# Kernel tuning notes

Measured on AMD Instinct MI355X. Metric: run time of the kernel, lower is better.

## Reference

```python
import jax, jax.numpy as jnp
import numpy as np

HIDDEN = 2560
NUM_HEADS = 80
HEAD_DIM = 64
STATE = 128
N_GROUPS = 1
CONV_K = 4
CHUNK = 256
INTER = 2 * HIDDEN                       # 5120 = NUM_HEADS * HEAD_DIM
CONV_DIM = INTER + 2 * N_GROUPS * STATE  # 5376
PROJ = INTER + CONV_DIM + NUM_HEADS      # 10576
EPS = 1e-5
DT_MIN, DT_MAX = 0.0, 100.0


def segment_sum(x):
    # x: (..., T) -> (..., T, T); out[i, j] = sum_{j < k <= i} x[k], -inf above diag
    T = x.shape[-1]
    xe = jnp.broadcast_to(x[..., :, None], x.shape + (T,))  # [i, j] = x[i]
    mask_lo = jnp.tril(jnp.ones((T, T), dtype=bool), -1)
    seg = jnp.cumsum(jnp.where(mask_lo, xe, 0.0), axis=-2)
    mask = jnp.tril(jnp.ones((T, T), dtype=bool), 0)
    return jnp.where(mask, seg, -jnp.inf)


def setup_inputs() -> dict:
    key = jax.random.key(0)
    k0, k1, k2, k3 = jax.random.split(key, 4)
    x = jax.random.normal(k0, (2, 2048, HIDDEN), jnp.float32)
    in_proj_w = jax.random.normal(k1, (PROJ, HIDDEN), jnp.float32) * (HIDDEN ** -0.5)
    conv1d_w = jax.random.normal(k2, (CONV_DIM, CONV_K), jnp.float32) * (CONV_K ** -0.5)
    conv1d_b = jnp.zeros((CONV_DIM,), jnp.float32)
    A_log = jnp.log(jnp.arange(1, NUM_HEADS + 1, dtype=jnp.float32))
    D = jnp.ones((NUM_HEADS,), jnp.float32)
    dt_bias = jnp.ones((NUM_HEADS,), jnp.float32)
    norm_weight = jnp.ones((INTER,), jnp.float32)
    out_proj_w = jax.random.normal(k3, (HIDDEN, INTER), jnp.float32) * (INTER ** -0.5)
    return dict(input_states=x, in_proj_w=in_proj_w, conv1d_w=conv1d_w,
                conv1d_b=conv1d_b, A_log=A_log, D=D, dt_bias=dt_bias,
                norm_weight=norm_weight, out_proj_w=out_proj_w)


def _mamba2_forward(input_states, in_proj_w, conv1d_w, conv1d_b, A_log, D,
                    dt_bias, norm_weight, out_proj_w):
    b, s, _ = input_states.shape
    proj = input_states @ in_proj_w.T                       # (b, s, PROJ)
    gate, hs, dt = jnp.split(proj, [INTER, INTER + CONV_DIM], axis=-1)

    # causal depthwise conv1d + SiLU
    xT = jnp.transpose(hs, (0, 2, 1))                       # (b, conv_dim, s)
    xT = jnp.pad(xT, ((0, 0), (0, 0), (CONV_K - 1, 0)))
    conv = jax.lax.conv_general_dilated(
        xT, conv1d_w[:, None, :], (1,), 'VALID',
        feature_group_count=CONV_DIM, dimension_numbers=('NCH', 'OIH', 'NCH'))
    hs = jax.nn.silu(jnp.transpose(conv + conv1d_b[None, :, None], (0, 2, 1)))

    hs, B, C = jnp.split(hs, [INTER, INTER + N_GROUPS * STATE], axis=-1)
    A = -jnp.exp(A_log)                                     # (h,)
    dt = jnp.clip(jax.nn.softplus(dt + dt_bias), DT_MIN, DT_MAX)  # (b, s, h)

    X = hs.reshape(b, s, NUM_HEADS, HEAD_DIM)
    rep = NUM_HEADS // N_GROUPS
    B = jnp.repeat(B.reshape(b, s, N_GROUPS, STATE), rep, axis=2)
    C = jnp.repeat(C.reshape(b, s, N_GROUPS, STATE), rep, axis=2)

    pad = (-s) % CHUNK
    D_res = D[None, None, :, None] * jnp.pad(X, ((0, 0), (0, pad), (0, 0), (0, 0)))
    Xd = X * dt[..., None]                                  # discretized input
    dA = A[None, None, :] * dt                              # (b, s, h)

    def chunk(t):
        t = jnp.pad(t, [(0, 0), (0, pad)] + [(0, 0)] * (t.ndim - 2))
        return t.reshape(t.shape[0], -1, CHUNK, *t.shape[2:])

    Xc, Bc, Cc = chunk(Xd), chunk(B), chunk(C)              # (b, c, l, h, ...)
    Ac = jnp.transpose(chunk(dA), (0, 3, 1, 2))             # (b, h, c, l)
    A_cum = jnp.cumsum(Ac, axis=-1)

    # 1. intra-chunk (diagonal block) outputs
    L = jnp.exp(segment_sum(Ac))                            # (b, h, c, l, l)
    G = jnp.einsum('bclhn,bcshn->bhcls', Cc, Bc)
    Y_diag = jnp.einsum('bhcls,bcshp->bclhp', G * L, Xc)

    # 2. per-chunk final states
    decay_states = jnp.exp(A_cum[..., -1:] - A_cum)         # (b, h, c, l)
    states = jnp.einsum('bclhn,bhcl,bclhp->bchpn', Bc, decay_states, Xc)

    # 3. inter-chunk recurrence
    A_last = A_cum[..., -1]                                 # (b, h, c)
    decay_chunk = jnp.exp(segment_sum(jnp.pad(A_last, ((0, 0), (0, 0), (1, 0)))))
    states = jnp.concatenate([jnp.zeros_like(states[:, :1]), states], axis=1)
    new_states = jnp.einsum('bhzc,bchpn->bzhpn', decay_chunk, states)
    states = new_states[:, :-1]                             # (b, c, h, p, n)

    # 4. state -> output conversion
    Y_off = jnp.einsum('bclhn,bchpn,bhcl->bclhp', Cc, states, jnp.exp(A_cum))

    y = (Y_diag + Y_off).reshape(b, -1, NUM_HEADS, HEAD_DIM) + D_res
    y = y[:, :s].reshape(b, s, INTER)

    # gated RMSNorm
    y = y * jax.nn.silu(gate)
    var = jnp.mean(y * y, axis=-1, keepdims=True)
    y = y * jax.lax.rsqrt(var + EPS) * norm_weight
    return y @ out_proj_w.T


def reference(input_states, in_proj_w, conv1d_w, conv1d_b, A_log, D, dt_bias,
              norm_weight, out_proj_w):
    return _mamba2_forward(input_states, in_proj_w, conv1d_w, conv1d_b, A_log,
                           D, dt_bias, norm_weight, out_proj_w)
```

## Files before the change

kernel.cpp:

```cpp
#include <hip/hip_runtime.h>
#include <hip/hip_bf16.h>
#include <math.h>

#define HIDDEN   2560
#define NUM_HEADS 80
#define HEAD_DIM 64
#define STATE    128
#define CONV_K   4
#define CHUNK    256
#define INTER    (2*HIDDEN)
#define CONV_DIM (INTER + 2*STATE)
#define PROJ     (INTER + CONV_DIM + NUM_HEADS)
#define PROJ_PAD 10240
#define NBC      336
#define NBCP     384
#define EPS      1e-5f

#define BATCH 2
#define SEQ   2048
#define TOK   (BATCH*SEQ)
#define NC    (SEQ/CHUNK)
#define KSPL2 8
#define KCH2  (HIDDEN/KSPL2)

typedef __attribute__((ext_vector_type(8))) short bf16x8;
typedef __attribute__((ext_vector_type(4))) float f32x4;

#define MFMA16(a,b,c) __builtin_amdgcn_mfma_f32_16x16x32_bf16((a),(b),(c),0,0,0)

__device__ __forceinline__ unsigned short f2bf(float f){
    union{float f;unsigned u;}v; v.f=f;
    unsigned r = v.u + 0x7fffu + ((v.u>>16)&1u);
    return (unsigned short)(r>>16);
}
__device__ __forceinline__ float bf2f(unsigned short s){
    union{unsigned u;float f;}v; v.u = ((unsigned)s)<<16; return v.f;
}
__device__ __forceinline__ void unpack8(uint4 u, float* e){
    e[0]=bf2f((unsigned short)(u.x&0xffff)); e[1]=bf2f((unsigned short)(u.x>>16));
    e[2]=bf2f((unsigned short)(u.y&0xffff)); e[3]=bf2f((unsigned short)(u.y>>16));
    e[4]=bf2f((unsigned short)(u.z&0xffff)); e[5]=bf2f((unsigned short)(u.z>>16));
    e[6]=bf2f((unsigned short)(u.w&0xffff)); e[7]=bf2f((unsigned short)(u.w>>16));
}

__device__ __forceinline__ void gld16(const void* g, void* l){
    __builtin_amdgcn_global_load_lds((const __attribute__((address_space(1))) void*)g,
                                     (__attribute__((address_space(3))) void*)l, 16, 0, 0);
}

template<bool BF16OUT>
__global__ __launch_bounds__(256) void gemm_bf16(const unsigned short* __restrict__ A, int lda,
                                                 const unsigned short* __restrict__ B, int ldb,
                                                 void* __restrict__ Cv, int ldc, int K) {
    __shared__ unsigned short As[128][64];
    __shared__ unsigned short Bs[128][64];
    int tid = threadIdx.x;
    int lane = tid & 63, wid = tid >> 6;
    int wr = wid >> 1, wc = wid & 1;

    int bm, bn;
    if ((gridDim.y & 7) == 0) {
        int bid   = blockIdx.y * gridDim.x + blockIdx.x;
        int xcd   = bid & 7;
        int local = bid >> 3;
        int mrows = gridDim.y >> 3;
        bm = (xcd * mrows + (local % mrows)) * 128;
        bn = (local / mrows) * 128;
    } else {
        bm = blockIdx.y * 128;
        bn = blockIdx.x * 128;
    }

    f32x4 acc[4][4];
    #pragma unroll
    for (int i=0;i<4;i++)
        #pragma unroll
        for (int j=0;j<4;j++) acc[i][j] = (f32x4){0.f,0.f,0.f,0.f};

    int srow_off = lane >> 3;
    int sslot    = lane & 7;

    for (int k0 = 0; k0 < K; k0 += 64) {
        #pragma unroll
        for (int q=0;q<4;q++){
            int brow = (wid*4+q)*8;
            int row  = brow + srow_off;
            int sl   = sslot ^ (row & 7);
            gld16(A + (size_t)(bm + row)*lda + k0 + sl*8, &As[brow][0]);
            gld16(B + (size_t)(bn + row)*ldb + k0 + sl*8, &Bs[brow][0]);
        }
        __syncthreads();
        #pragma unroll
        for (int kk=0; kk<64; kk+=32){
            bf16x8 a[4], b[4];
            #pragma unroll
            for (int i=0;i<4;i++){
                int row = wr*64 + i*16 + (lane&15);
                int slot = ((kk>>3) + (lane>>4)) ^ (row & 7);
                a[i] = *(const bf16x8*)&As[row][slot*8];
            }
            #pragma unroll
            for (int j=0;j<4;j++){
                int row = wc*64 + j*16 + (lane&15);
                int slot = ((kk>>3) + (lane>>4)) ^ (row & 7);
                b[j] = *(const bf16x8*)&Bs[row][slot*8];
            }
            #pragma unroll
            for (int i=0;i<4;i++)
                #pragma unroll
                for (int j=0;j<4;j++)
                    acc[i][j] = MFMA16(a[i], b[j], acc[i][j]);
        }
        __syncthreads();
    }
    #pragma unroll
    for (int i=0;i<4;i++){
        int row0 = bm + wr*64 + i*16 + (lane>>4)*4;
        #pragma unroll
        for (int j=0;j<4;j++){
            int col = bn + wc*64 + j*16 + (lane&15);
            #pragma unroll
            for (int r=0;r<4;r++){
                if (BF16OUT)
                    ((unsigned short*)Cv)[(size_t)(row0+r)*ldc + col] = f2bf(acc[i][j][r]);
                else
                    ((float*)Cv)[(size_t)(row0+r)*ldc + col] = acc[i][j][r];
            }
        }
    }
}

__global__ __launch_bounds__(256) void bc_splitk_mfma(const unsigned short* __restrict__ xhi,
                                                      const unsigned short* __restrict__ xlo,
                                                      const unsigned short* __restrict__ whi,
                                                      const unsigned short* __restrict__ wlo,
                                                      float* __restrict__ Cpart) {
    __shared__ unsigned short As[128][64];
    __shared__ unsigned short Bs[128][64];
    int tid = threadIdx.x;
    int lane = tid & 63, wid = tid >> 6;
    int wr = wid >> 1, wc = wid & 1;
    int bn = blockIdx.x * 128, bm = blockIdx.y * 128, z = blockIdx.z;

    f32x4 acc[4][4];
    #pragma unroll
    for (int i=0;i<4;i++)
        #pragma unroll
        for (int j=0;j<4;j++) acc[i][j] = (f32x4){0.f,0.f,0.f,0.f};

    int srow_off = lane >> 3;
    int sslot    = lane & 7;

    for (int term = 0; term < 3; ++term){
        const unsigned short* A = (term==2) ? xlo : xhi;
        const unsigned short* B = (term==0) ? wlo : whi;
        for (int k0 = z*KCH2; k0 < z*KCH2 + KCH2; k0 += 64) {
            #pragma unroll
            for (int q=0;q<4;q++){
                int brow = (wid*4+q)*8;
                int row  = brow + srow_off;
                int sl   = sslot ^ (row & 7);
                gld16(A + (size_t)(bm + row)*HIDDEN + k0 + sl*8, &As[brow][0]);
                gld16(B + (size_t)(bn + row)*HIDDEN + k0 + sl*8, &Bs[brow][0]);
            }
            __syncthreads();
            #pragma unroll
            for (int kk=0; kk<64; kk+=32){
                bf16x8 a[4], b[4];
                #pragma unroll
                for (int i=0;i<4;i++){
                    int row = wr*64 + i*16 + (lane&15);
                    int slot = ((kk>>3) + (lane>>4)) ^ (row & 7);
                    a[i] = *(const bf16x8*)&As[row][slot*8];
                }
                #pragma unroll
                for (int j=0;j<4;j++){
                    int row = wc*64 + j*16 + (lane&15);
                    int slot = ((kk>>3) + (lane>>4)) ^ (row & 7);
                    b[j] = *(const bf16x8*)&Bs[row][slot*8];
                }
                #pragma unroll
                for (int i=0;i<4;i++)
                    #pragma unroll
                    for (int j=0;j<4;j++)
                        acc[i][j] = MFMA16(a[i], b[j], acc[i][j]);
            }
            __syncthreads();
        }
    }
    float* Cz = Cpart + (size_t)z*TOK*NBCP;
    #pragma unroll
    for (int i=0;i<4;i++){
        int row0 = bm + wr*64 + i*16 + (lane>>4)*4;
        #pragma unroll
        for (int j=0;j<4;j++){
            int col = bn + wc*64 + j*16 + (lane&15);
            #pragma unroll
            for (int r=0;r<4;r++)
                Cz[(size_t)(row0+r)*NBCP + col] = acc[i][j][r];
        }
    }
}

__global__ __launch_bounds__(256) void reduce_bc2(const float* __restrict__ part,
                                                  const float* __restrict__ dt_bias,
                                                  float* __restrict__ outBC,
                                                  float* __restrict__ dtbuf) {
    size_t i4 = (size_t)blockIdx.x*256 + threadIdx.x;
    if (i4 >= (size_t)TOK*NBCP/4) return;
    size_t i = i4*4;
    float4 s = *(const float4*)(part + i);
    #pragma unroll
    for (int z=1; z<KSPL2; z++){
        float4 v = *(const float4*)(part + (size_t)z*TOK*NBCP + i);
        s.x += v.x; s.y += v.y; s.z += v.z; s.w += v.w;
    }
    int col = (int)(i % NBCP);
    int t   = (int)(i / NBCP);
    if (col < 256) {
        *(float4*)(outBC + (size_t)t*NBC + col) = s;
    } else if (col < NBC) {
        int h = col - 256;
        float e[4] = {s.x, s.y, s.z, s.w};
        #pragma unroll
        for (int u=0;u<4;u++){
            float xv = e[u] + dt_bias[h+u];
            float sp = (xv > 20.f) ? xv : log1pf(expf(xv));
            e[u] = fminf(fmaxf(sp, 0.f), 100.f);
        }
        float4 o; o.x=e[0]; o.y=e[1]; o.z=e[2]; o.w=e[3];
        *(float4*)(dtbuf + (size_t)t*NUM_HEADS + h) = o;
    }
}

#define N4A ((size_t)TOK*HIDDEN/4)
#define N4B ((size_t)PROJ_PAD*HIDDEN/4)
#define N4C ((size_t)NBCP*HIDDEN/4)
__global__ __launch_bounds__(256) void prep_kernel(const float* __restrict__ x,
                                                   const float* __restrict__ in_w,
                                                   unsigned short* __restrict__ xhi,
                                                   unsigned short* __restrict__ xlo,
                                                   unsigned short* __restrict__ w1b,
                                                   unsigned short* __restrict__ wbc_hi,
                                                   unsigned short* __restrict__ wbc_lo) {
    size_t gid = (size_t)blockIdx.x*256 + threadIdx.x;
    if (gid < N4A) {
        size_t i = gid*4;
        float4 v = *(const float4*)(x + i);
        float e[4] = {v.x, v.y, v.z, v.w};
        ushort4 h, l;
        unsigned short* hp = (unsigned short*)&h;
        unsigned short* lp = (unsigned short*)&l;
        #pragma unroll
        for (int u=0;u<4;u++){
            unsigned short hv = f2bf(e[u]);
            hp[u] = hv;
            lp[u] = f2bf(e[u] - bf2f(hv));
        }
        *(ushort4*)(xhi + i) = h;
        *(ushort4*)(xlo + i) = l;
    } else if (gid < N4A + N4B) {
        size_t i = (gid - N4A)*4;
        float4 v = *(const float4*)(in_w + i);
        ushort4 o;
        o.x=f2bf(v.x); o.y=f2bf(v.y); o.z=f2bf(v.z); o.w=f2bf(v.w);
        *(ushort4*)(w1b + i) = o;
    } else {
        size_t j = gid - N4A - N4B;
        size_t i = j*4;
        int row = (int)(i / HIDDEN);
        int kk  = (int)(i % HIDDEN);
        ushort4 h, l;
        h.x=h.y=h.z=h.w=0; l.x=l.y=l.z=l.w=0;
        if (row < NBC){
            float4 v = *(const float4*)(in_w + (size_t)(2*INTER + row)*HIDDEN + kk);
            float e[4] = {v.x, v.y, v.z, v.w};
            unsigned short* hp = (unsigned short*)&h;
            unsigned short* lp = (unsigned short*)&l;
            #pragma unroll
            for (int u=0;u<4;u++){
                unsigned short hv = f2bf(e[u]);
                hp[u] = hv;
                lp[u] = f2bf(e[u] - bf2f(hv));
            }
        }
        *(ushort4*)(wbc_hi + i) = h;
        *(ushort4*)(wbc_lo + i) = l;
    }
}

#define XBLK ((TOK/64)*(INTER/64))
#define W2BLK ((int)(((size_t)HIDDEN*INTER/4)/256))
__global__ __launch_bounds__(256) void conv_fused(const unsigned short* __restrict__ projb,
                                                  const float* __restrict__ projBC,
                                                  const float* __restrict__ cw,
                                                  const float* __restrict__ cb,
                                                  const float* __restrict__ out_w,
                                                  unsigned short* __restrict__ XT,
                                                  float* __restrict__ xBC_BC,
                                                  unsigned short* __restrict__ BT,
                                                  unsigned short* __restrict__ Cb,
                                                  unsigned short* __restrict__ w2b) {
    __shared__ unsigned short raw[68][66];
    int bid = blockIdx.x;
    int tid = threadIdx.x;
    if (bid < XBLK) {
        int bx = bid & 63, by = bid >> 6;
        int t0 = bx * 64, d0 = by * 64;
        int b  = t0 / SEQ;
        int s0 = t0 % SEQ;
        for (int f = tid; f < 67*8; f += 256){
            int r = f >> 3, g = f & 7;
            int sp = s0 - 3 + r;
            uint4 v;
            if (sp >= 0) v = *(const uint4*)(projb + ((size_t)(b*SEQ+sp))*PROJ_PAD + INTER + d0 + g*8);
            else { v.x=0u; v.y=0u; v.z=0u; v.w=0u; }
            unsigned int* dst = (unsigned int*)&raw[r][g*8];
            dst[0]=v.x; dst[1]=v.y; dst[2]=v.z; dst[3]=v.w;
        }
        __syncthreads();
        int t = tid & 63, dg = tid >> 6;
        #pragma unroll
        for (int dd = 0; dd < 16; dd++){
            int d = dg*16 + dd;
            float acc = cb[d0+d];
            #pragma unroll
            for (int j=0;j<CONV_K;j++)
                acc += cw[(d0+d)*CONV_K+j] * bf2f(raw[t+j][d]);
            float val = acc/(1.f+expf(-acc));
            XT[((size_t)(b*INTER + d0 + d))*SEQ + s0 + t] = f2bf(val);
        }
    } else if (bid < XBLK + TOK) {
        int idx = (bid - XBLK)*256 + tid;
        int d = idx & 255;
        int t = idx >> 8;
        int b = t / SEQ, sl = t % SEQ;
        int dc = INTER + d;
        float acc = cb[dc];
        #pragma unroll
        for (int j=0;j<CONV_K;j++){
            int sp = sl - (CONV_K-1) + j;
            if (sp >= 0)
                acc += cw[dc*CONV_K+j] * projBC[((size_t)(b*SEQ+sp))*NBC + d];
        }
        float val = acc / (1.f + expf(-acc));
        xBC_BC[(size_t)t*256 + d] = val;
        if (d < 128)
            BT[((size_t)(b*128 + d))*SEQ + sl] = f2bf(val);
        else
            Cb[(size_t)t*128 + (d-128)] = f2bf(val);
    } else {
        size_t i4 = (size_t)(bid - XBLK - TOK)*256 + tid;
        size_t i = i4*4;
        float4 v = *(const float4*)(out_w + i);
        ushort4 o; o.x=f2bf(v.x); o.y=f2bf(v.y); o.z=f2bf(v.z); o.w=f2bf(v.w);
        *(ushort4*)(w2b + i) = o;
    }
}

__global__ __launch_bounds__(256) void cumsum_kernel(const float* __restrict__ dtbuf,
                                                     const float* __restrict__ A_log,
                                                     float* __restrict__ A_cum) {
    int c = blockIdx.x, h = blockIdx.y, b = blockIdx.z;
    int l = threadIdx.x;
    float A = -expf(A_log[h]);
    float v = A * dtbuf[(size_t)(b*SEQ + c*CHUNK + l)*NUM_HEADS + h];
    __shared__ float buf[CHUNK];
    buf[l] = v;
    __syncthreads();
    for (int off=1; off<CHUNK; off<<=1){
        float t = (l>=off) ? buf[l-off] : 0.f;
        __syncthreads();
        buf[l] += t;
        __syncthreads();
    }
    A_cum[((size_t)b*NUM_HEADS + h)*SEQ + c*CHUNK + l] = buf[l];
}

__global__ __launch_bounds__(256) void g_kernel(const float* __restrict__ xBC_BC,
                                                unsigned short* __restrict__ G) {
    int c = blockIdx.x, p = blockIdx.y, b = blockIdx.z;
    int lt = 0, a0 = 0;
    while (a0 + lt + 1 <= p) { a0 += lt + 1; lt++; }
    int st = p - a0;
    int l0 = lt*32, s0 = st*32;
    __shared__ float Cs[32][132];
    __shared__ float Bs[32][132];
    int tid = threadIdx.x, ty = tid >> 4, tx = tid & 15;
    float acc[2][2];
    acc[0][0]=0.f; acc[0][1]=0.f; acc[1][0]=0.f; acc[1][1]=0.f;

    size_t rowC = ((size_t)(b*SEQ + c*CHUNK + l0))*256 + 128;
    size_t rowB = ((size_t)(b*SEQ + c*CHUNK + s0))*256;
    #pragma unroll
    for (int it=0; it<4; it++){
        int f = tid + it*256;
        int r = f >> 5, c4 = f & 31;
        *(float4*)&Cs[r][c4*4] = *(const float4*)(xBC_BC + rowC + (size_t)r*256 + c4*4);
        *(float4*)&Bs[r][c4*4] = *(const float4*)(xBC_BC + rowB + (size_t)r*256 + c4*4);
    }
    __syncthreads();
    #pragma unroll 8
    for (int k=0;k<128;k++){
        float a0v = Cs[ty*2][k],   a1v = Cs[ty*2+1][k];
        float b0v = Bs[tx*2][k],   b1v = Bs[tx*2+1][k];
        acc[0][0] += a0v*b0v; acc[0][1] += a0v*b1v;
        acc[1][0] += a1v*b0v; acc[1][1] += a1v*b1v;
    }
    size_t Gb = ((size_t)(b*NC + c)) << 16;
    #pragma unroll
    for (int i=0;i<2;i++){
        ushort2 g2;
        g2.x = f2bf(acc[i][0]); g2.y = f2bf(acc[i][1]);
        *(ushort2*)(G + Gb + (size_t)(l0 + ty*2 + i)*256 + s0 + tx*2) = g2;
    }
}

__global__ __launch_bounds__(256) void states_mfma(const unsigned short* __restrict__ XT,
                                                   const unsigned short* __restrict__ BT,
                                                   const float* __restrict__ dtbuf,
                                                   const float* __restrict__ A_cum,
                                                   unsigned short* __restrict__ statesT) {
    int c = blockIdx.x, h = blockIdx.y, b = blockIdx.z;
    __shared__ unsigned short Asx[64][64];
    __shared__ unsigned short Bs[128][64];
    __shared__ float wl[CHUNK];
    int tid = threadIdx.x, lane = tid & 63, wid = tid >> 6;
    {
        const float* ac = A_cum + ((size_t)(b*NUM_HEADS+h))*SEQ + c*CHUNK;
        float Alast = ac[CHUNK-1];
        wl[tid] = expf(Alast - ac[tid]) * dtbuf[((size_t)(b*SEQ + c*CHUNK + tid))*NUM_HEADS + h];
    }
    __syncthreads();
    f32x4 acc[4][2];
    #pragma unroll
    for (int i=0;i<4;i++)
        #pragma unroll
        for (int j=0;j<2;j++) acc[i][j] = (f32x4){0.f,0.f,0.f,0.f};

    for (int kc = 0; kc < 4; kc++){
        int lbase = kc*64;
        #pragma unroll
        for (int q=0;q<4;q++){
            int brow = (wid*4+q)*8;
            int row  = brow + (lane>>3);
            int sl   = (lane&7) ^ (row & 7);
            gld16(BT + ((size_t)(b*128 + row))*SEQ + c*CHUNK + lbase + sl*8, &Bs[brow][0]);
        }
        #pragma unroll
        for (int it=0; it<2; it++){
            int f = tid + it*256;
            int r = f >> 3, g = f & 7;
            uint4 v = *(const uint4*)(XT + ((size_t)(b*INTER + h*HEAD_DIM + r))*SEQ + c*CHUNK + lbase + g*8);
            float e[8]; unpack8(v, e);
            unsigned short o[8];
            #pragma unroll
            for (int u=0;u<8;u++) o[u] = f2bf(e[u] * wl[lbase + g*8 + u]);
            int slot = g ^ (r & 7);
            *(ushort4*)&Asx[r][slot*8]   = *(ushort4*)&o[0];
            *(ushort4*)&Asx[r][slot*8+4] = *(ushort4*)&o[4];
        }
        __syncthreads();
        #pragma unroll
        for (int kk=0; kk<64; kk+=32){
            bf16x8 a[4], bb[2];
            #pragma unroll
            for (int i=0;i<4;i++){
                int row = i*16 + (lane&15);
                int slot = ((kk>>3)+(lane>>4)) ^ (row&7);
                a[i] = *(const bf16x8*)&Asx[row][slot*8];
            }
            #pragma unroll
            for (int j=0;j<2;j++){
                int row = wid*32 + j*16 + (lane&15);
                int slot = ((kk>>3)+(lane>>4)) ^ (row&7);
                bb[j] = *(const bf16x8*)&Bs[row][slot*8];
            }
            #pragma unroll
            for (int i=0;i<4;i++)
                #pragma unroll
                for (int j=0;j<2;j++)
                    acc[i][j] = MFMA16(a[i], bb[j], acc[i][j]);
        }
        __syncthreads();
    }
    size_t sb = ((size_t)((b*NC + c)*NUM_HEADS + h))*(HEAD_DIM*STATE);
    #pragma unroll
    for (int i=0;i<4;i++){
        #pragma unroll
        for (int j=0;j<2;j++){
            int n = wid*32 + j*16 + (lane&15);
            int p0 = i*16 + (lane>>4)*4;
            #pragma unroll
            for (int r=0;r<4;r++)
                statesT[sb + (size_t)(p0+r)*128 + n] = f2bf(acc[i][j][r]);
        }
    }
}

__global__ __launch_bounds__(256) void recur_kernel(const float* __restrict__ A_cum,
                                                    unsigned short* __restrict__ states) {
    int h = blockIdx.x, b = blockIdx.y, z = blockIdx.z;
    int tid = threadIdx.x;
    float Srun[8];
    #pragma unroll
    for (int i=0;i<8;i++) Srun[i]=0.f;
    const float* acum = A_cum + ((size_t)b*NUM_HEADS + h)*SEQ;
    for (int c=0;c<NC;c++){
        float alast = acum[c*CHUNK + CHUNK-1];
        float dec = expf(alast);
        size_t base = ((size_t)((b*NC + c)*NUM_HEADS + h))*(HEAD_DIM*STATE);
        #pragma unroll
        for (int i=0;i<8;i++){
            size_t idx = base + (size_t)tid + (size_t)(z*8+i)*256;
            float raw = bf2f(states[idx]);
            states[idx] = f2bf(Srun[i]);
            Srun[i] = Srun[i]*dec + raw;
        }
    }
}

__global__ __launch_bounds__(256) void yscan_mfma(const unsigned short* __restrict__ G,
                                                  const unsigned short* __restrict__ Cb,
                                                  const unsigned short* __restrict__ XT,
                                                  const float* __restrict__ dtbuf,
                                                  const float* __restrict__ A_cum,
                                                  const unsigned short* __restrict__ statesT,
                                                  const float* __restrict__ Dvec,
                                                  unsigned short* __restrict__ projb) {
    int xb = blockIdx.x;
    int c = xb & 7, lt = xb >> 3;
    int h = blockIdx.y, b = blockIdx.z;
    int l0 = lt*64;
    __shared__ __align__(16) char pool[32768];
    unsigned short (*Cs)[128] = (unsigned short(*)[128])pool;
    unsigned short (*St)[128] = (unsigned short(*)[128])(pool + 16384);
    unsigned short (*Gw)[64]  = (unsigned short(*)[64])pool;
    unsigned short (*Xs)[64]  = (unsigned short(*)[64])(pool + 8192);
    float (*Ot)[68]           = (float(*)[68])pool;
    __shared__ float ac[CHUNK], dts[CHUNK];
    int tid = threadIdx.x, lane = tid & 63, wid = tid >> 6;
    ac[tid]  = A_cum[((size_t)(b*NUM_HEADS + h))*SEQ + c*CHUNK + tid];
    dts[tid] = dtbuf[((size_t)(b*SEQ + c*CHUNK + tid))*NUM_HEADS + h];

    size_t stb = ((size_t)((b*NC + c)*NUM_HEADS + h))*(HEAD_DIM*STATE);
    #pragma unroll
    for (int q=0;q<4;q++){
        int brow = (wid*4+q)*4;
        int row  = brow + (lane>>4);
        int sl   = (lane&15) ^ (row & 7);
        gld16(Cb + ((size_t)(b*SEQ + c*CHUNK + l0 + row))*128 + sl*8, &Cs[brow][0]);
        gld16(statesT + stb + (size_t)row*128 + sl*8, &St[brow][0]);
    }
    __syncthreads();

    f32x4 acc1[4];
    #pragma unroll
    for (int j=0;j<4;j++) acc1[j] = (f32x4){0.f,0.f,0.f,0.f};
    #pragma unroll
    for (int kk=0; kk<128; kk+=32){
        int arow = wid*16 + (lane&15);
        int aslot = ((kk>>3)+(lane>>4)) ^ (arow&7);
        bf16x8 a = *(const bf16x8*)&Cs[arow][aslot*8];
        #pragma unroll
        for (int j=0;j<4;j++){
            int brow = j*16 + (lane&15);
            int bslot = ((kk>>3)+(lane>>4)) ^ (brow&7);
            bf16x8 bb = *(const bf16x8*)&St[brow][bslot*8];
            acc1[j] = MFMA16(a, bb, acc1[j]);
        }
    }
    float el[4];
    #pragma unroll
    for (int r=0;r<4;r++) el[r] = expf(ac[l0 + wid*16 + (lane>>4)*4 + r]);
    float master[4][4];
    #pragma unroll
    for (int j=0;j<4;j++)
        #pragma unroll
        for (int r=0;r<4;r++) master[j][r] = acc1[j][r]*el[r];
    __syncthreads();

    size_t Gb = ((size_t)(b*NC + c)) << 16;
    f32x4 acc2[4];
    #pragma unroll
    for (int j=0;j<4;j++) acc2[j] = (f32x4){0.f,0.f,0.f,0.f};
    for (int st=0; st<=lt; st++){
        int s0 = st*64;
        #pragma unroll
        for (int it=0; it<2; it++){
            int f = tid + it*256;
            int r = f >> 3, g = f & 7;
            uint4 v = *(const uint4*)(G + Gb + (size_t)(l0 + r)*256 + s0 + g*8);
            float e[8]; unpack8(v, e);
            float acl = ac[l0 + r];
            unsigned short o[8];
            #pragma unroll
            for (int u=0;u<8;u++){
                int s = s0 + g*8 + u;
                float w = (s <= l0 + r) ? expf(acl - ac[s])*dts[s] : 0.f;
                o[u] = f2bf(e[u]*w);
            }
            int slot = g ^ (r&7);
            *(ushort4*)&Gw[r][slot*8]   = *(ushort4*)&o[0];
            *(ushort4*)&Gw[r][slot*8+4] = *(ushort4*)&o[4];
        }
        #pragma unroll
        for (int q=0;q<2;q++){
            int brow = (wid*2+q)*8;
            int row  = brow + (lane>>3);
            int sl   = (lane&7) ^ (row&7);
            gld16(XT + ((size_t)(b*INTER + h*HEAD_DIM + row))*SEQ + c*CHUNK + s0 + sl*8,
                  &Xs[brow][0]);
        }
        __syncthreads();
        #pragma unroll
        for (int kk=0; kk<64; kk+=32){
            int arow = wid*16 + (lane&15);
            int aslot = ((kk>>3)+(lane>>4)) ^ (arow&7);
            bf16x8 a = *(const bf16x8*)&Gw[arow][aslot*8];
            #pragma unroll
            for (int j=0;j<4;j++){
                int brow = j*16 + (lane&15);
                int bslot = ((kk>>3)+(lane>>4)) ^ (brow&7);
                bf16x8 bb = *(const bf16x8*)&Xs[brow][bslot*8];
                acc2[j] = MFMA16(a, bb, acc2[j]);
            }
        }
        if (st < lt) __syncthreads();
    }

    float Dh = Dvec[h];
    #pragma unroll
    for (int j=0;j<4;j++){
        int p = j*16 + (lane&15);
        #pragma unroll
        for (int r=0;r<4;r++){
            int sl_ = wid*16 + (lane>>4)*4 + r;
            int slot = (sl_>>3) ^ (p&7);
            float xv = bf2f(Xs[p][slot*8 + (sl_&7)]);
            master[j][r] += acc2[j][r] + Dh*xv;
        }
    }
    __syncthreads();

    #pragma unroll
    for (int j=0;j<4;j++){
        int p = j*16 + (lane&15);
        #pragma unroll
        for (int r=0;r<4;r++)
            Ot[wid*16 + (lane>>4)*4 + r][p] = master[j][r];
    }
    __syncthreads();
    #pragma unroll
    for (int it=0; it<4; it++){
        int f = tid + it*256;
        int r = f >> 4, c4 = f & 15;
        ushort4 o;
        o.x = f2bf(Ot[r][c4*4+0]); o.y = f2bf(Ot[r][c4*4+1]);
        o.z = f2bf(Ot[r][c4*4+2]); o.w = f2bf(Ot[r][c4*4+3]);
        *(ushort4*)(projb + ((size_t)(b*SEQ + c*CHUNK + l0 + r))*PROJ_PAD + INTER + h*HEAD_DIM + c4*4) = o;
    }
}

__global__ __launch_bounds__(256) void gate_norm_kernel(const unsigned short* __restrict__ projb,
                                                        const float* __restrict__ normw,
                                                        unsigned short* __restrict__ yb) {
    int t = blockIdx.x;
    int tid = threadIdx.x;
    const unsigned short* row = projb + (size_t)t*PROJ_PAD;
    __shared__ float red[4];
    float vals[20];
    float ss = 0.f;
    #pragma unroll
    for (int i=0;i<5;i++){
        int j = (tid + i*256)*4;
        ushort4 g4 = *(const ushort4*)(row + j);
        ushort4 y4 = *(const ushort4*)(row + INTER + j);
        #pragma unroll
        for (int u=0;u<4;u++){
            float g = bf2f(((const unsigned short*)&g4)[u]);
            float y = bf2f(((const unsigned short*)&y4)[u]);
            float gv = g / (1.f + expf(-g));
            float v = y * gv;
            vals[i*4+u] = v;
            ss += v*v;
        }
    }
    #pragma unroll
    for (int off=32; off; off>>=1) ss += __shfl_xor(ss, off);
    if ((tid&63)==0) red[tid>>6] = ss;
    __syncthreads();
    float tot = red[0]+red[1]+red[2]+red[3];
    float inv = rsqrtf(tot/(float)INTER + EPS);
    #pragma unroll
    for (int i=0;i<5;i++){
        int j = (tid + i*256)*4;
        ushort4 o;
        o.x = f2bf(vals[i*4+0] * inv * normw[j+0]);
        o.y = f2bf(vals[i*4+1] * inv * normw[j+1]);
        o.z = f2bf(vals[i*4+2] * inv * normw[j+2]);
        o.w = f2bf(vals[i*4+3] * inv * normw[j+3]);
        *(ushort4*)(yb + (size_t)t*INTER + j) = o;
    }
}

extern "C" void kernel_launch(void* const* d_in, const int* in_sizes, int n_in,
                              void* d_out, int out_size, void* d_ws, size_t ws_size,
                              hipStream_t stream) {
    const float* x        = (const float*)d_in[0];
    const float* in_w     = (const float*)d_in[1];
    const float* conv_w   = (const float*)d_in[2];
    const float* conv_b   = (const float*)d_in[3];
    const float* A_log    = (const float*)d_in[4];
    const float* Dvec     = (const float*)d_in[5];
    const float* dt_bias  = (const float*)d_in[6];
    const float* norm_w   = (const float*)d_in[7];
    const float* out_w    = (const float*)d_in[8];
    float* out = (float*)d_out;
    (void)ws_size; (void)n_in; (void)in_sizes; (void)out_size;

    const size_t PROJB   = (size_t)TOK*PROJ_PAD*2;
    const size_t PROJBCB = (size_t)TOK*NBC*4;
    const size_t XTB     = (size_t)TOK*INTER*2;
    const size_t XBCBCB  = (size_t)TOK*256*4;
    const size_t BTB     = (size_t)BATCH*128*SEQ*2;
    const size_t CBB     = (size_t)TOK*128*2;
    const size_t GBYTES  = (size_t)BATCH*NC*CHUNK*CHUNK*2;
    const size_t DTB     = (size_t)TOK*NUM_HEADS*4;
    const size_t ACUMB   = DTB;
    const size_t STB     = (size_t)BATCH*NC*NUM_HEADS*HEAD_DIM*STATE*2;
    const size_t XHB   = (size_t)TOK*HIDDEN*2;
    const size_t WBCB  = (size_t)NBCP*HIDDEN*2;
    const size_t YBB   = (size_t)TOK*INTER*2;

    char* base = (char*)d_ws;
    size_t off = 0;
    unsigned short* projb  = (unsigned short*)(base + off); off += PROJB;
    float* projBC          = (float*)(base + off);          off += PROJBCB;
    unsigned short* XTp    = (unsigned short*)(base + off); off += XTB;
    float* xBC_BC          = (float*)(base + off);          off += XBCBCB;
    unsigned short* BTp    = (unsigned short*)(base + off); off += BTB;
    unsigned short* Cbp    = (unsigned short*)(base + off); off += CBB;
    unsigned short* Gp     = (unsigned short*)(base + off); off += GBYTES;
    float* dtbuf           = (float*)(base + off);          off += DTB;
    float* A_cum           = (float*)(base + off);          off += ACUMB;
    unsigned short* statesT= (unsigned short*)(base + off); off += STB;
    char*  T               = base + off;
    unsigned short* xhi    = (unsigned short*)T;
    unsigned short* xlo    = (unsigned short*)(T + XHB);
    unsigned short* wbc_hi = (unsigned short*)(T + 2*XHB);
    unsigned short* wbc_lo = (unsigned short*)(T + 2*XHB + WBCB);
    unsigned short* w1b    = (unsigned short*)(T + 2*XHB + 2*WBCB);
    float* bcpart          = (float*)w1b;
    unsigned short* yb     = (unsigned short*)T;
    unsigned short* w2b    = (unsigned short*)(T + YBB);

    {
        unsigned total_blocks = (unsigned)((N4A + N4B + N4C) / 256);
        prep_kernel<<<total_blocks, 256, 0, stream>>>(x, in_w, xhi, xlo, w1b, wbc_hi, wbc_lo);
    }
    gemm_bf16<true><<<dim3(PROJ_PAD/128, TOK/128), 256, 0, stream>>>(xhi, HIDDEN, w1b, HIDDEN,
                                                                     projb, PROJ_PAD, HIDDEN);
    bc_splitk_mfma<<<dim3(NBCP/128, TOK/128, KSPL2), 256, 0, stream>>>(xhi, xlo, wbc_hi, wbc_lo, bcpart);
    reduce_bc2<<<(unsigned)(((size_t)TOK*NBCP/4)/256), 256, 0, stream>>>(bcpart, dt_bias, projBC, dtbuf);
    conv_fused<<<XBLK + TOK + W2BLK, 256, 0, stream>>>(projb, projBC, conv_w, conv_b, out_w,
                                                       XTp, xBC_BC, BTp, Cbp, w2b);
    cumsum_kernel<<<dim3(NC, NUM_HEADS, BATCH), 256, 0, stream>>>(dtbuf, A_log, A_cum);
    g_kernel<<<dim3(NC, 36, BATCH), 256, 0, stream>>>(xBC_BC, Gp);
    states_mfma<<<dim3(NC, NUM_HEADS, BATCH), 256, 0, stream>>>(XTp, BTp, dtbuf, A_cum, statesT);
    recur_kernel<<<dim3(NUM_HEADS, BATCH, 4), 256, 0, stream>>>(A_cum, statesT);
    yscan_mfma<<<dim3(NC*4, NUM_HEADS, BATCH), 256, 0, stream>>>(Gp, Cbp, XTp, dtbuf, A_cum,
                                                                 statesT, Dvec, projb);
    gate_norm_kernel<<<TOK, 256, 0, stream>>>(projb, norm_w, yb);
    gemm_bf16<false><<<dim3(HIDDEN/128, TOK/128), 256, 0, stream>>>(yb, INTER, w2b, INTER,
                                                                    out, HIDDEN, INTER);
}
```

Measured before the change: 710.3 us.

## Merge independent pipeline stages into horizontally fused mega-kernels

Combines independent kernels into shared launches that branch on block index: the main in-projection GEMM with the split-K BC GEMM, the split-K reduction with the conv over the x channels, the BC conv with the cumsum and the out-weight conversion, and the states computation with the G kernel. The GEMM1 epilogue now stages output tiles through shared memory so the stores are coalesced 16-byte writes. This cuts launch count and lets small kernels fill the tail of larger ones. The cost is heavier, branchy kernels whose register and LDS use is set by the largest branch, which may lower occupancy.

```diff
diff --git a/kernel.cpp b/kernel.cpp
--- a/kernel.cpp
+++ b/kernel.cpp
@@ -23,37 +23,183 @@
 #define KSPL2 8
 #define KCH2  (HIDDEN/KSPL2)
 
+#define G1_BLOCKS 2560
+#define BC_BLOCKS 768
+#define RED_BLOCKS 1536
+#define CXT_BLOCKS 5120
+#define CBC_BLOCKS 4096
+#define CUM_BLOCKS 1280
+#define W2_BLOCKS  12800
+#define ST_BLOCKS  1280
+#define GK_BLOCKS  576
+
 typedef __attribute__((ext_vector_type(8))) short bf16x8;
 typedef __attribute__((ext_vector_type(4))) float f32x4;
+typedef unsigned short us;
 
 #define MFMA16(a,b,c) __builtin_amdgcn_mfma_f32_16x16x32_bf16((a),(b),(c),0,0,0)
 
-__device__ __forceinline__ unsigned short f2bf(float f){
+__device__ __forceinline__ us f2bf(float f){
     union{float f;unsigned u;}v; v.f=f;
     unsigned r = v.u + 0x7fffu + ((v.u>>16)&1u);
-    return (unsigned short)(r>>16);
-}
-__device__ __forceinline__ float bf2f(unsigned short s){
+    return (us)(r>>16);
+}
+__device__ __forceinline__ float bf2f(us s){
     union{unsigned u;float f;}v; v.u = ((unsigned)s)<<16; return v.f;
 }
 __device__ __forceinline__ void unpack8(uint4 u, float* e){
-    e[0]=bf2f((unsigned short)(u.x&0xffff)); e[1]=bf2f((unsigned short)(u.x>>16));
-    e[2]=bf2f((unsigned short)(u.y&0xffff)); e[3]=bf2f((unsigned short)(u.y>>16));
-    e[4]=bf2f((unsigned short)(u.z&0xffff)); e[5]=bf2f((unsigned short)(u.z>>16));
-    e[6]=bf2f((unsigned short)(u.w&0xffff)); e[7]=bf2f((unsigned short)(u.w>>16));
-}
-
+    e[0]=bf2f((us)(u.x&0xffff)); e[1]=bf2f((us)(u.x>>16));
+    e[2]=bf2f((us)(u.y&0xffff)); e[3]=bf2f((us)(u.y>>16));
+    e[4]=bf2f((us)(u.z&0xffff)); e[5]=bf2f((us)(u.z>>16));
+    e[6]=bf2f((us)(u.w&0xffff)); e[7]=bf2f((us)(u.w>>16));
+}
 __device__ __forceinline__ void gld16(const void* g, void* l){
     __builtin_amdgcn_global_load_lds((const __attribute__((address_space(1))) void*)g,
                                      (__attribute__((address_space(3))) void*)l, 16, 0, 0);
 }
 
+__global__ __launch_bounds__(256) void mega_gemm1_bc(const us* __restrict__ xhi,
+                                                     const us* __restrict__ xlo,
+                                                     const us* __restrict__ w1b,
+                                                     const us* __restrict__ wbc_hi,
+                                                     const us* __restrict__ wbc_lo,
+                                                     us* __restrict__ projb,
+                                                     float* __restrict__ Cpart) {
+    __shared__ __align__(16) char SH[32768];
+    us (*As)[64] = (us(*)[64])SH;
+    us (*Bs)[64] = (us(*)[64])(SH + 16384);
+    int bid = blockIdx.x;
+    int tid = threadIdx.x;
+    int lane = tid & 63, wid = tid >> 6;
+    int wr = wid >> 1, wc = wid & 1;
+    int srow_off = lane >> 3;
+    int sslot    = lane & 7;
+
+    f32x4 acc[4][4];
+    #pragma unroll
+    for (int i=0;i<4;i++)
+        #pragma unroll
+        for (int j=0;j<4;j++) acc[i][j] = (f32x4){0.f,0.f,0.f,0.f};
+
+    if (bid < G1_BLOCKS) {
+        int xcd = bid & 7, local = bid >> 3;
+        int bm = (xcd*4 + (local & 3))*128;
+        int bn = (local >> 2)*128;
+        for (int k0 = 0; k0 < HIDDEN; k0 += 64) {
+            #pragma unroll
+            for (int q=0;q<4;q++){
+                int brow = (wid*4+q)*8;
+                int row  = brow + srow_off;
+                int sl   = sslot ^ (row & 7);
+                gld16(xhi + (size_t)(bm + row)*HIDDEN + k0 + sl*8, &As[brow][0]);
+                gld16(w1b + (size_t)(bn + row)*HIDDEN + k0 + sl*8, &Bs[brow][0]);
+            }
+            __syncthreads();
+            #pragma unroll
+            for (int kk=0; kk<64; kk+=32){
+                bf16x8 a[4], b[4];
+                #pragma unroll
+                for (int i=0;i<4;i++){
+                    int row = wr*64 + i*16 + (lane&15);
+                    int slot = ((kk>>3) + (lane>>4)) ^ (row & 7);
+                    a[i] = *(const bf16x8*)&As[row][slot*8];
+                }
+                #pragma unroll
+                for (int j=0;j<4;j++){
+                    int row = wc*64 + j*16 + (lane&15);
+                    int slot = ((kk>>3) + (lane>>4)) ^ (row & 7);
+                    b[j] = *(const bf16x8*)&Bs[row][slot*8];
+                }
+                #pragma unroll
+                for (int i=0;i<4;i++)
+                    #pragma unroll
+                    for (int j=0;j<4;j++)
+                        acc[i][j] = MFMA16(a[i], b[j], acc[i][j]);
+            }
+            __syncthreads();
+        }
+        us (*Ct)[128] = (us(*)[128])SH;
+        #pragma unroll
+        for (int i=0;i<4;i++){
+            int r0 = wr*64 + i*16 + (lane>>4)*4;
+            #pragma unroll
+            for (int j=0;j<4;j++){
+                int cc = wc*64 + j*16 + (lane&15);
+                #pragma unroll
+                for (int r=0;r<4;r++)
+                    Ct[r0+r][cc] = f2bf(acc[i][j][r]);
+            }
+        }
+        __syncthreads();
+        #pragma unroll
+        for (int it=0; it<8; it++){
+            int f = tid + it*256;
+            int row = f >> 4, ch = f & 15;
+            *(uint4*)(projb + (size_t)(bm+row)*PROJ_PAD + bn + ch*8) = *(uint4*)&Ct[row][ch*8];
+        }
+    } else {
+        int b2 = bid - G1_BLOCKS;
+        int bn = (b2 % 3)*128;
+        int bm = ((b2/3) & 31)*128;
+        int z  = b2 / 96;
+        for (int term = 0; term < 3; ++term){
+            const us* A = (term==2) ? xlo : xhi;
+            const us* B = (term==0) ? wbc_lo : wbc_hi;
+            for (int k0 = z*KCH2; k0 < z*KCH2 + KCH2; k0 += 64) {
+                #pragma unroll
+                for (int q=0;q<4;q++){
+                    int brow = (wid*4+q)*8;
+                    int row  = brow + srow_off;
+                    int sl   = sslot ^ (row & 7);
+                    gld16(A + (size_t)(bm + row)*HIDDEN + k0 + sl*8, &As[brow][0]);
+                    gld16(B + (size_t)(bn + row)*HIDDEN + k0 + sl*8, &Bs[brow][0]);
+                }
+                __syncthreads();
+                #pragma unroll
+                for (int kk=0; kk<64; kk+=32){
+                    bf16x8 a[4], b[4];
+                    #pragma unroll
+                    for (int i=0;i<4;i++){
+                        int row = wr*64 + i*16 + (lane&15);
+                        int slot = ((kk>>3) + (lane>>4)) ^ (row & 7);
+                        a[i] = *(const bf16x8*)&As[row][slot*8];
+                    }
+                    #pragma unroll
+                    for (int j=0;j<4;j++){
+                        int row = wc*64 + j*16 + (lane&15);
+                        int slot = ((kk>>3) + (lane>>4)) ^ (row & 7);
+                        b[j] = *(const bf16x8*)&Bs[row][slot*8];
+                    }
+                    #pragma unroll
+                    for (int i=0;i<4;i++)
+                        #pragma unroll
+                        for (int j=0;j<4;j++)
+                            acc[i][j] = MFMA16(a[i], b[j], acc[i][j]);
+                }
+                __syncthreads();
+            }
+        }
+        float* Cz = Cpart + (size_t)z*TOK*NBCP;
+        #pragma unroll
+        for (int i=0;i<4;i++){
+            int row0 = bm + wr*64 + i*16 + (lane>>4)*4;
+            #pragma unroll
+            for (int j=0;j<4;j++){
+                int col = bn + wc*64 + j*16 + (lane&15);
+                #pragma unroll
+                for (int r=0;r<4;r++)
+                    Cz[(size_t)(row0+r)*NBCP + col] = acc[i][j][r];
+            }
+        }
+    }
+}
+
 template<bool BF16OUT>
-__global__ __launch_bounds__(256) void gemm_bf16(const unsigned short* __restrict__ A, int lda,
-                                                 const unsigned short* __restrict__ B, int ldb,
+__global__ __launch_bounds__(256) void gemm_bf16(const us* __restrict__ A, int lda,
+                                                 const us* __restrict__ B, int ldb,
                                                  void* __restrict__ Cv, int ldc, int K) {
-    __shared__ unsigned short As[128][64];
-    __shared__ unsigned short Bs[128][64];
+    __shared__ us As[128][64];
+    __shared__ us Bs[128][64];
     int tid = threadIdx.x;
     int lane = tid & 63, wid = tid >> 6;
     int wr = wid >> 1, wc = wid & 1;
@@ -122,114 +268,11 @@
             #pragma unroll
             for (int r=0;r<4;r++){
                 if (BF16OUT)
-                    ((unsigned short*)Cv)[(size_t)(row0+r)*ldc + col] = f2bf(acc[i][j][r]);
+                    ((us*)Cv)[(size_t)(row0+r)*ldc + col] = f2bf(acc[i][j][r]);
                 else
                     ((float*)Cv)[(size_t)(row0+r)*ldc + col] = acc[i][j][r];
             }
         }
-    }
-}
-
-__global__ __launch_bounds__(256) void bc_splitk_mfma(const unsigned short* __restrict__ xhi,
-                                                      const unsigned short* __restrict__ xlo,
-                                                      const unsigned short* __restrict__ whi,
-                                                      const unsigned short* __restrict__ wlo,
-                                                      float* __restrict__ Cpart) {
-    __shared__ unsigned short As[128][64];
-    __shared__ unsigned short Bs[128][64];
-    int tid = threadIdx.x;
-    int lane = tid & 63, wid = tid >> 6;
-    int wr = wid >> 1, wc = wid & 1;
-    int bn = blockIdx.x * 128, bm = blockIdx.y * 128, z = blockIdx.z;
-
-    f32x4 acc[4][4];
-    #pragma unroll
-    for (int i=0;i<4;i++)
-        #pragma unroll
-        for (int j=0;j<4;j++) acc[i][j] = (f32x4){0.f,0.f,0.f,0.f};
-
-    int srow_off = lane >> 3;
-    int sslot    = lane & 7;
-
-    for (int term = 0; term < 3; ++term){
-        const unsigned short* A = (term==2) ? xlo : xhi;
-        const unsigned short* B = (term==0) ? wlo : whi;
-        for (int k0 = z*KCH2; k0 < z*KCH2 + KCH2; k0 += 64) {
-            #pragma unroll
-            for (int q=0;q<4;q++){
-                int brow = (wid*4+q)*8;
-                int row  = brow + srow_off;
-                int sl   = sslot ^ (row & 7);
-                gld16(A + (size_t)(bm + row)*HIDDEN + k0 + sl*8, &As[brow][0]);
-                gld16(B + (size_t)(bn + row)*HIDDEN + k0 + sl*8, &Bs[brow][0]);
-            }
-            __syncthreads();
-            #pragma unroll
-            for (int kk=0; kk<64; kk+=32){
-                bf16x8 a[4], b[4];
-                #pragma unroll
-                for (int i=0;i<4;i++){
-                    int row = wr*64 + i*16 + (lane&15);
-                    int slot = ((kk>>3) + (lane>>4)) ^ (row & 7);
-                    a[i] = *(const bf16x8*)&As[row][slot*8];
-                }
-                #pragma unroll
-                for (int j=0;j<4;j++){
-                    int row = wc*64 + j*16 + (lane&15);
-                    int slot = ((kk>>3) + (lane>>4)) ^ (row & 7);
-                    b[j] = *(const bf16x8*)&Bs[row][slot*8];
-                }
-                #pragma unroll
-                for (int i=0;i<4;i++)
-                    #pragma unroll
-                    for (int j=0;j<4;j++)
-                        acc[i][j] = MFMA16(a[i], b[j], acc[i][j]);
-            }
-            __syncthreads();
-        }
-    }
-    float* Cz = Cpart + (size_t)z*TOK*NBCP;
-    #pragma unroll
-    for (int i=0;i<4;i++){
-        int row0 = bm + wr*64 + i*16 + (lane>>4)*4;
-        #pragma unroll
-        for (int j=0;j<4;j++){
-            int col = bn + wc*64 + j*16 + (lane&15);
-            #pragma unroll
-            for (int r=0;r<4;r++)
-                Cz[(size_t)(row0+r)*NBCP + col] = acc[i][j][r];
-        }
-    }
-}
-
-__global__ __launch_bounds__(256) void reduce_bc2(const float* __restrict__ part,
-                                                  const float* __restrict__ dt_bias,
-                                                  float* __restrict__ outBC,
-                                                  float* __restrict__ dtbuf) {
-    size_t i4 = (size_t)blockIdx.x*256 + threadIdx.x;
-    if (i4 >= (size_t)TOK*NBCP/4) return;
-    size_t i = i4*4;
-    float4 s = *(const float4*)(part + i);
-    #pragma unroll
-    for (int z=1; z<KSPL2; z++){
-        float4 v = *(const float4*)(part + (size_t)z*TOK*NBCP + i);
-        s.x += v.x; s.y += v.y; s.z += v.z; s.w += v.w;
-    }
-    int col = (int)(i % NBCP);
-    int t   = (int)(i / NBCP);
-    if (col < 256) {
-        *(float4*)(outBC + (size_t)t*NBC + col) = s;
-    } else if (col < NBC) {
-        int h = col - 256;
-        float e[4] = {s.x, s.y, s.z, s.w};
-        #pragma unroll
-        for (int u=0;u<4;u++){
-            float xv = e[u] + dt_bias[h+u];
-            float sp = (xv > 20.f) ? xv : log1pf(expf(xv));
-            e[u] = fminf(fmaxf(sp, 0.f), 100.f);
-        }
-        float4 o; o.x=e[0]; o.y=e[1]; o.z=e[2]; o.w=e[3];
-        *(float4*)(dtbuf + (size_t)t*NUM_HEADS + h) = o;
     }
 }
 
@@ -238,22 +281,22 @@
 #define N4C ((size_t)NBCP*HIDDEN/4)
 __global__ __launch_bounds__(256) void prep_kernel(const float* __restrict__ x,
                                                    const float* __restrict__ in_w,
-                                                   unsigned short* __restrict__ xhi,
-                                                   unsigned short* __restrict__ xlo,
-                                                   unsigned short* __restrict__ w1b,
-                                                   unsigned short* __restrict__ wbc_hi,
-                                                   unsigned short* __restrict__ wbc_lo) {
+                                                   us* __restrict__ xhi,
+                                                   us* __restrict__ xlo,
+                                                   us* __restrict__ w1b,
+                                                   us* __restrict__ wbc_hi,
+                                                   us* __restrict__ wbc_lo) {
     size_t gid = (size_t)blockIdx.x*256 + threadIdx.x;
     if (gid < N4A) {
         size_t i = gid*4;
         float4 v = *(const float4*)(x + i);
         float e[4] = {v.x, v.y, v.z, v.w};
         ushort4 h, l;
-        unsigned short* hp = (unsigned short*)&h;
-        unsigned short* lp = (unsigned short*)&l;
+        us* hp = (us*)&h;
+        us* lp = (us*)&l;
         #pragma unroll
         for (int u=0;u<4;u++){
-            unsigned short hv = f2bf(e[u]);
+            us hv = f2bf(e[u]);
             hp[u] = hv;
             lp[u] = f2bf(e[u] - bf2f(hv));
         }
@@ -275,11 +318,11 @@
         if (row < NBC){
             float4 v = *(const float4*)(in_w + (size_t)(2*INTER + row)*HIDDEN + kk);
             float e[4] = {v.x, v.y, v.z, v.w};
-            unsigned short* hp = (unsigned short*)&h;
-            unsigned short* lp = (unsigned short*)&l;
+            us* hp = (us*)&h;
+            us* lp = (us*)&l;
             #pragma unroll
             for (int u=0;u<4;u++){
-                unsigned short hv = f2bf(e[u]);
+                us hv = f2bf(e[u]);
                 hp[u] = hv;
                 lp[u] = f2bf(e[u] - bf2f(hv));
             }
@@ -289,23 +332,45 @@
     }
 }
 
-#define XBLK ((TOK/64)*(INTER/64))
-#define W2BLK ((int)(((size_t)HIDDEN*INTER/4)/256))
-__global__ __launch_bounds__(256) void conv_fused(const unsigned short* __restrict__ projb,
-                                                  const float* __restrict__ projBC,
-                                                  const float* __restrict__ cw,
-                                                  const float* __restrict__ cb,
-                                                  const float* __restrict__ out_w,
-                                                  unsigned short* __restrict__ XT,
-                                                  float* __restrict__ xBC_BC,
-                                                  unsigned short* __restrict__ BT,
-                                                  unsigned short* __restrict__ Cb,
-                                                  unsigned short* __restrict__ w2b) {
-    __shared__ unsigned short raw[68][66];
+__global__ __launch_bounds__(256) void mega_red_convxt(const float* __restrict__ part,
+                                                       const float* __restrict__ dt_bias,
+                                                       const us* __restrict__ projb,
+                                                       const float* __restrict__ cw,
+                                                       const float* __restrict__ cb,
+                                                       float* __restrict__ outBC,
+                                                       float* __restrict__ dtbuf,
+                                                       us* __restrict__ XT) {
+    __shared__ us raw[68][66];
     int bid = blockIdx.x;
     int tid = threadIdx.x;
-    if (bid < XBLK) {
-        int bx = bid & 63, by = bid >> 6;
+    if (bid < RED_BLOCKS) {
+        size_t i4 = (size_t)bid*256 + tid;
+        size_t i = i4*4;
+        float4 s = *(const float4*)(part + i);
+        #pragma unroll
+        for (int z=1; z<KSPL2; z++){
+            float4 v = *(const float4*)(part + (size_t)z*TOK*NBCP + i);
+            s.x += v.x; s.y += v.y; s.z += v.z; s.w += v.w;
+        }
+        int col = (int)(i % NBCP);
+        int t   = (int)(i / NBCP);
+        if (col < 256) {
+            *(float4*)(outBC + (size_t)t*NBC + col) = s;
+        } else if (col < NBC) {
+            int h = col - 256;
+            float e[4] = {s.x, s.y, s.z, s.w};
+            #pragma unroll
+            for (int u=0;u<4;u++){
+                float xv = e[u] + dt_bias[h+u];
+                float sp = (xv > 20.f) ? xv : log1pf(expf(xv));
+                e[u] = fminf(fmaxf(sp, 0.f), 100.f);
+            }
+            float4 o; o.x=e[0]; o.y=e[1]; o.z=e[2]; o.w=e[3];
+            *(float4*)(dtbuf + (size_t)t*NUM_HEADS + h) = o;
+        }
+    } else {
+        int b3 = bid - RED_BLOCKS;
+        int bx = b3 & 63, by = b3 >> 6;
         int t0 = bx * 64, d0 = by * 64;
         int b  = t0 / SEQ;
         int s0 = t0 % SEQ;
@@ -330,8 +395,25 @@
             float val = acc/(1.f+expf(-acc));
             XT[((size_t)(b*INTER + d0 + d))*SEQ + s0 + t] = f2bf(val);
         }
-    } else if (bid < XBLK + TOK) {
-        int idx = (bid - XBLK)*256 + tid;
+    }
+}
+
+__global__ __launch_bounds__(256) void mega_convbc_cum_w2(const float* __restrict__ projBC,
+                                                          const float* __restrict__ cw,
+                                                          const float* __restrict__ cb,
+                                                          const float* __restrict__ dtbuf,
+                                                          const float* __restrict__ A_log,
+                                                          const float* __restrict__ out_w,
+                                                          float* __restrict__ xBC_BC,
+                                                          us* __restrict__ BT,
+                                                          us* __restrict__ Cb,
+                                                          float* __restrict__ A_cum,
+                                                          us* __restrict__ w2b) {
+    __shared__ float buf[CHUNK];
+    int bid = blockIdx.x;
+    int tid = threadIdx.x;
+    if (bid < CBC_BLOCKS) {
+        int idx = bid*256 + tid;
         int d = idx & 255;
         int t = idx >> 8;
         int b = t / SEQ, sl = t % SEQ;
@@ -349,8 +431,23 @@
             BT[((size_t)(b*128 + d))*SEQ + sl] = f2bf(val);
         else
             Cb[(size_t)t*128 + (d-128)] = f2bf(val);
+    } else if (bid < CBC_BLOCKS + CUM_BLOCKS) {
+        int b4 = bid - CBC_BLOCKS;
+        int c = b4 & 7, h = (b4 >> 3) % 80, b = b4 / 640;
+        int l = tid;
+        float A = -expf(A_log[h]);
+        float v = A * dtbuf[(size_t)(b*SEQ + c*CHUNK + l)*NUM_HEADS + h];
+        buf[l] = v;
+        __syncthreads();
+        for (int off=1; off<CHUNK; off<<=1){
+            float t2 = (l>=off) ? buf[l-off] : 0.f;
+            __syncthreads();
+            buf[l] += t2;
+            __syncthreads();
+        }
+        A_cum[((size_t)b*NUM_HEADS + h)*SEQ + c*CHUNK + l] = buf[l];
     } else {
-        size_t i4 = (size_t)(bid - XBLK - TOK)*256 + tid;
+        size_t i4 = (size_t)(bid - CBC_BLOCKS - CUM_BLOCKS)*256 + tid;
         size_t i = i4*4;
         float4 v = *(const float4*)(out_w + i);
         ushort4 o; o.x=f2bf(v.x); o.y=f2bf(v.y); o.z=f2bf(v.z); o.w=f2bf(v.w);
@@ -358,148 +455,134 @@
     }
 }
 
-__global__ __launch_bounds__(256) void cumsum_kernel(const float* __restrict__ dtbuf,
-                                                     const float* __restrict__ A_log,
-                                                     float* __restrict__ A_cum) {
-    int c = blockIdx.x, h = blockIdx.y, b = blockIdx.z;
-    int l = threadIdx.x;
-    float A = -expf(A_log[h]);
-    float v = A * dtbuf[(size_t)(b*SEQ + c*CHUNK + l)*NUM_HEADS + h];
-    __shared__ float buf[CHUNK];
-    buf[l] = v;
-    __syncthreads();
-    for (int off=1; off<CHUNK; off<<=1){
-        float t = (l>=off) ? buf[l-off] : 0.f;
+__global__ __launch_bounds__(256) void mega_states_g(const us* __restrict__ XT,
+                                                     const us* __restrict__ BT,
+                                                     const float* __restrict__ dtbuf,
+                                                     const float* __restrict__ A_cum,
+                                                     const float* __restrict__ xBC_BC,
+                                                     us* __restrict__ statesT,
+                                                     us* __restrict__ G) {
+    __shared__ __align__(16) char SH[33792];
+    int bid = blockIdx.x;
+    int tid = threadIdx.x;
+    if (bid < ST_BLOCKS) {
+        int c = bid & 7, h = (bid >> 3) % 80, b = bid / 640;
+        us (*Asx)[64] = (us(*)[64])SH;
+        us (*Bs)[64]  = (us(*)[64])(SH + 8192);
+        float* wl     = (float*)(SH + 24576);
+        int lane = tid & 63, wid = tid >> 6;
+        {
+            const float* ac = A_cum + ((size_t)(b*NUM_HEADS+h))*SEQ + c*CHUNK;
+            float Alast = ac[CHUNK-1];
+            wl[tid] = expf(Alast - ac[tid]) * dtbuf[((size_t)(b*SEQ + c*CHUNK + tid))*NUM_HEADS + h];
+        }
         __syncthreads();
-        buf[l] += t;
+        f32x4 acc[4][2];
+        #pragma unroll
+        for (int i=0;i<4;i++)
+            #pragma unroll
+            for (int j=0;j<2;j++) acc[i][j] = (f32x4){0.f,0.f,0.f,0.f};
+
+        for (int kc = 0; kc < 4; kc++){
+            int lbase = kc*64;
+            #pragma unroll
+            for (int q=0;q<4;q++){
+                int brow = (wid*4+q)*8;
+                int row  = brow + (lane>>3);
+                int sl   = (lane&7) ^ (row & 7);
+                gld16(BT + ((size_t)(b*128 + row))*SEQ + c*CHUNK + lbase + sl*8, &Bs[brow][0]);
+            }
+            #pragma unroll
+            for (int it=0; it<2; it++){
+                int f = tid + it*256;
+                int r = f >> 3, g = f & 7;
+                uint4 v = *(const uint4*)(XT + ((size_t)(b*INTER + h*HEAD_DIM + r))*SEQ + c*CHUNK + lbase + g*8);
+                float e[8]; unpack8(v, e);
+                us o[8];
+                #pragma unroll
+                for (int u=0;u<8;u++) o[u] = f2bf(e[u] * wl[lbase + g*8 + u]);
+                int slot = g ^ (r & 7);
+                *(ushort4*)&Asx[r][slot*8]   = *(ushort4*)&o[0];
+                *(ushort4*)&Asx[r][slot*8+4] = *(ushort4*)&o[4];
+            }
+            __syncthreads();
+            #pragma unroll
+            for (int kk=0; kk<64; kk+=32){
+                bf16x8 a[4], bb[2];
+                #pragma unroll
+                for (int i=0;i<4;i++){
+                    int row = i*16 + (lane&15);
+                    int slot = ((kk>>3)+(lane>>4)) ^ (row&7);
+                    a[i] = *(const bf16x8*)&Asx[row][slot*8];
+                }
+                #pragma unroll
+                for (int j=0;j<2;j++){
+                    int row = wid*32 + j*16 + (lane&15);
+                    int slot = ((kk>>3)+(lane>>4)) ^ (row&7);
+                    bb[j] = *(const bf16x8*)&Bs[row][slot*8];
+                }
+                #pragma unroll
+                for (int i=0;i<4;i++)
+                    #pragma unroll
+                    for (int j=0;j<2;j++)
+                        acc[i][j] = MFMA16(a[i], bb[j], acc[i][j]);
+            }
+            __syncthreads();
+        }
+        size_t sb = ((size_t)((b*NC + c)*NUM_HEADS + h))*(HEAD_DIM*STATE);
+        #pragma unroll
+        for (int i=0;i<4;i++){
+            #pragma unroll
+            for (int j=0;j<2;j++){
+                int n = wid*32 + j*16 + (lane&15);
+                int p0 = i*16 + (lane>>4)*4;
+                #pragma unroll
+                for (int r=0;r<4;r++)
+                    statesT[sb + (size_t)(p0+r)*128 + n] = f2bf(acc[i][j][r]);
+            }
+        }
+    } else {
+        int b5 = bid - ST_BLOCKS;
+        int c = b5 & 7, p = (b5 >> 3) % 36, b = b5 / 288;
+        int lt = 0, a0 = 0;
+        while (a0 + lt + 1 <= p) { a0 += lt + 1; lt++; }
+        int st = p - a0;
+        int l0 = lt*32, s0 = st*32;
+        float (*Cs)[132] = (float(*)[132])SH;
+        float (*Bs2)[132] = (float(*)[132])(SH + 16896);
+        int ty = tid >> 4, tx = tid & 15;
+        float acc[2][2];
+        acc[0][0]=0.f; acc[0][1]=0.f; acc[1][0]=0.f; acc[1][1]=0.f;
+
+        size_t rowC = ((size_t)(b*SEQ + c*CHUNK + l0))*256 + 128;
+        size_t rowB = ((size_t)(b*SEQ + c*CHUNK + s0))*256;
+        #pragma unroll
+        for (int it=0; it<4; it++){
+            int f = tid + it*256;
+            int r = f >> 5, c4 = f & 31;
+            *(float4*)&Cs[r][c4*4]  = *(const float4*)(xBC_BC + rowC + (size_t)r*256 + c4*4);
+            *(float4*)&Bs2[r][c4*4] = *(const float4*)(xBC_BC + rowB + (size_t)r*256 + c4*4);
+        }
         __syncthreads();
-    }
-    A_cum[((size_t)b*NUM_HEADS + h)*SEQ + c*CHUNK + l] = buf[l];
-}
-
-__global__ __launch_bounds__(256) void g_kernel(const float* __restrict__ xBC_BC,
-                                                unsigned short* __restrict__ G) {
-    int c = blockIdx.x, p = blockIdx.y, b = blockIdx.z;
-    int lt = 0, a0 = 0;
-    while (a0 + lt + 1 <= p) { a0 += lt + 1; lt++; }
-    int st = p - a0;
-    int l0 = lt*32, s0 = st*32;
-    __shared__ float Cs[32][132];
-    __shared__ float Bs[32][132];
-    int tid = threadIdx.x, ty = tid >> 4, tx = tid & 15;
-    float acc[2][2];
-    acc[0][0]=0.f; acc[0][1]=0.f; acc[1][0]=0.f; acc[1][1]=0.f;
-
-    size_t rowC = ((size_t)(b*SEQ + c*CHUNK + l0))*256 + 128;
-    size_t rowB = ((size_t)(b*SEQ + c*CHUNK + s0))*256;
-    #pragma unroll
-    for (int it=0; it<4; it++){
-        int f = tid + it*256;
-        int r = f >> 5, c4 = f & 31;
-        *(float4*)&Cs[r][c4*4] = *(const float4*)(xBC_BC + rowC + (size_t)r*256 + c4*4);
-        *(float4*)&Bs[r][c4*4] = *(const float4*)(xBC_BC + rowB + (size_t)r*256 + c4*4);
-    }
-    __syncthreads();
-    #pragma unroll 8
-    for (int k=0;k<128;k++){
-        float a0v = Cs[ty*2][k],   a1v = Cs[ty*2+1][k];
-        float b0v = Bs[tx*2][k],   b1v = Bs[tx*2+1][k];
-        acc[0][0] += a0v*b0v; acc[0][1] += a0v*b1v;
-        acc[1][0] += a1v*b0v; acc[1][1] += a1v*b1v;
-    }
-    size_t Gb = ((size_t)(b*NC + c)) << 16;
-    #pragma unroll
-    for (int i=0;i<2;i++){
-        ushort2 g2;
-        g2.x = f2bf(acc[i][0]); g2.y = f2bf(acc[i][1]);
-        *(ushort2*)(G + Gb + (size_t)(l0 + ty*2 + i)*256 + s0 + tx*2) = g2;
-    }
-}
-
-__global__ __launch_bounds__(256) void states_mfma(const unsigned short* __restrict__ XT,
-                                                   const unsigned short* __restrict__ BT,
-                                                   const float* __restrict__ dtbuf,
-                                                   const float* __restrict__ A_cum,
-                                                   unsigned short* __restrict__ statesT) {
-    int c = blockIdx.x, h = blockIdx.y, b = blockIdx.z;
-    __shared__ unsigned short Asx[64][64];
-    __shared__ unsigned short Bs[128][64];
-    __shared__ float wl[CHUNK];
-    int tid = threadIdx.x, lane = tid & 63, wid = tid >> 6;
-    {
-        const float* ac = A_cum + ((size_t)(b*NUM_HEADS+h))*SEQ + c*CHUNK;
-        float Alast = ac[CHUNK-1];
-        wl[tid] = expf(Alast - ac[tid]) * dtbuf[((size_t)(b*SEQ + c*CHUNK + tid))*NUM_HEADS + h];
-    }
-    __syncthreads();
-    f32x4 acc[4][2];
-    #pragma unroll
-    for (int i=0;i<4;i++)
-        #pragma unroll
-        for (int j=0;j<2;j++) acc[i][j] = (f32x4){0.f,0.f,0.f,0.f};
-
-    for (int kc = 0; kc < 4; kc++){
-        int lbase = kc*64;
-        #pragma unroll
-        for (int q=0;q<4;q++){
-            int brow = (wid*4+q)*8;
-            int row  = brow + (lane>>3);
-            int sl   = (lane&7) ^ (row & 7);
-            gld16(BT + ((size_t)(b*128 + row))*SEQ + c*CHUNK + lbase + sl*8, &Bs[brow][0]);
-        }
-        #pragma unroll
-        for (int it=0; it<2; it++){
-            int f = tid + it*256;
-            int r = f >> 3, g = f & 7;
-            uint4 v = *(const uint4*)(XT + ((size_t)(b*INTER + h*HEAD_DIM + r))*SEQ + c*CHUNK + lbase + g*8);
-            float e[8]; unpack8(v, e);
-            unsigned short o[8];
-            #pragma unroll
-            for (int u=0;u<8;u++) o[u] = f2bf(e[u] * wl[lbase + g*8 + u]);
-            int slot = g ^ (r & 7);
-            *(ushort4*)&Asx[r][slot*8]   = *(ushort4*)&o[0];
-            *(ushort4*)&Asx[r][slot*8+4] = *(ushort4*)&o[4];
-        }
-        __syncthreads();
-        #pragma unroll
-        for (int kk=0; kk<64; kk+=32){
-            bf16x8 a[4], bb[2];
-            #pragma unroll
-            for (int i=0;i<4;i++){
-                int row = i*16 + (lane&15);
-                int slot = ((kk>>3)+(lane>>4)) ^ (row&7);
-                a[i] = *(const bf16x8*)&Asx[row][slot*8];
-            }
-            #pragma unroll
-            for (int j=0;j<2;j++){
-                int row = wid*32 + j*16 + (lane&15);
-                int slot = ((kk>>3)+(lane>>4)) ^ (row&7);
-                bb[j] = *(const bf16x8*)&Bs[row][slot*8];
-            }
-            #pragma unroll
-            for (int i=0;i<4;i++)
-                #pragma unroll
-                for (int j=0;j<2;j++)
-                    acc[i][j] = MFMA16(a[i], bb[j], acc[i][j]);
-        }
-        __syncthreads();
-    }
-    size_t sb = ((size_t)((b*NC + c)*NUM_HEADS + h))*(HEAD_DIM*STATE);
-    #pragma unroll
-    for (int i=0;i<4;i++){
-        #pragma unroll
-        for (int j=0;j<2;j++){
-            int n = wid*32 + j*16 + (lane&15);
-            int p0 = i*16 + (lane>>4)*4;
-            #pragma unroll
-            for (int r=0;r<4;r++)
-                statesT[sb + (size_t)(p0+r)*128 + n] = f2bf(acc[i][j][r]);
+        #pragma unroll 8
+        for (int k=0;k<128;k++){
+            float a0v = Cs[ty*2][k],   a1v = Cs[ty*2+1][k];
+            float b0v = Bs2[tx*2][k],  b1v = Bs2[tx*2+1][k];
+            acc[0][0] += a0v*b0v; acc[0][1] += a0v*b1v;
+            acc[1][0] += a1v*b0v; acc[1][1] += a1v*b1v;
+        }
+        size_t Gb = ((size_t)(b*NC + c)) << 16;
+        #pragma unroll
+        for (int i=0;i<2;i++){
+            ushort2 g2;
+            g2.x = f2bf(acc[i][0]); g2.y = f2bf(acc[i][1]);
+            *(ushort2*)(G + Gb + (size_t)(l0 + ty*2 + i)*256 + s0 + tx*2) = g2;
         }
     }
 }
 
 __global__ __launch_bounds__(256) void recur_kernel(const float* __restrict__ A_cum,
-                                                    unsigned short* __restrict__ states) {
+                                                    us* __restrict__ states) {
     int h = blockIdx.x, b = blockIdx.y, z = blockIdx.z;
     int tid = threadIdx.x;
     float Srun[8];
@@ -520,24 +603,24 @@
     }
 }
 
-__global__ __launch_bounds__(256) void yscan_mfma(const unsigned short* __restrict__ G,
-                                                  const unsigned short* __restrict__ Cb,
-                                                  const unsigned short* __restrict__ XT,
+__global__ __launch_bounds__(256) void yscan_mfma(const us* __restrict__ G,
+                                                  const us* __restrict__ Cb,
+                                                  const us* __restrict__ XT,
                                                   const float* __restrict__ dtbuf,
                                                   const float* __restrict__ A_cum,
-                                                  const unsigned short* __restrict__ statesT,
+                                                  const us* __restrict__ statesT,
                                                   const float* __restrict__ Dvec,
-                                                  unsigned short* __restrict__ projb) {
+                                                  us* __restrict__ projb) {
     int xb = blockIdx.x;
     int c = xb & 7, lt = xb >> 3;
     int h = blockIdx.y, b = blockIdx.z;
     int l0 = lt*64;
     __shared__ __align__(16) char pool[32768];
-    unsigned short (*Cs)[128] = (unsigned short(*)[128])pool;
-    unsigned short (*St)[128] = (unsigned short(*)[128])(pool + 16384);
-    unsigned short (*Gw)[64]  = (unsigned short(*)[64])pool;
-    unsigned short (*Xs)[64]  = (unsigned short(*)[64])(pool + 8192);
-    float (*Ot)[68]           = (float(*)[68])pool;
+    us (*Cs)[128] = (us(*)[128])pool;
+    us (*St)[128] = (us(*)[128])(pool + 16384);
+    us (*Gw)[64]  = (us(*)[64])pool;
+    us (*Xs)[64]  = (us(*)[64])(pool + 8192);
+    float (*Ot)[68] = (float(*)[68])pool;
     __shared__ float ac[CHUNK], dts[CHUNK];
     int tid = threadIdx.x, lane = tid & 63, wid = tid >> 6;
     ac[tid]  = A_cum[((size_t)(b*NUM_HEADS + h))*SEQ + c*CHUNK + tid];
@@ -593,7 +676,7 @@
             uint4 v = *(const uint4*)(G + Gb + (size_t)(l0 + r)*256 + s0 + g*8);
             float e[8]; unpack8(v, e);
             float acl = ac[l0 + r];
-            unsigned short o[8];
+            us o[8];
             #pragma unroll
             for (int u=0;u<8;u++){
                 int s = s0 + g*8 + u;
@@ -662,12 +745,12 @@
     }
 }
 
-__global__ __launch_bounds__(256) void gate_norm_kernel(const unsigned short* __restrict__ projb,
+__global__ __launch_bounds__(256) void gate_norm_kernel(const us* __restrict__ projb,
                                                         const float* __restrict__ normw,
-                                                        unsigned short* __restrict__ yb) {
+                                                        us* __restrict__ yb) {
     int t = blockIdx.x;
     int tid = threadIdx.x;
-    const unsigned short* row = projb + (size_t)t*PROJ_PAD;
+    const us* row = projb + (size_t)t*PROJ_PAD;
     __shared__ float red[4];
     float vals[20];
     float ss = 0.f;
@@ -678,8 +761,8 @@
         ushort4 y4 = *(const ushort4*)(row + INTER + j);
         #pragma unroll
         for (int u=0;u<4;u++){
-            float g = bf2f(((const unsigned short*)&g4)[u]);
-            float y = bf2f(((const unsigned short*)&y4)[u]);
+            float g = bf2f(((const us*)&g4)[u]);
+            float y = bf2f(((const us*)&y4)[u]);
             float gv = g / (1.f + expf(-g));
             float v = y * gv;
             vals[i*4+u] = v;
@@ -735,39 +818,39 @@
 
     char* base = (char*)d_ws;
     size_t off = 0;
-    unsigned short* projb  = (unsigned short*)(base + off); off += PROJB;
-    float* projBC          = (float*)(base + off);          off += PROJBCB;
-    unsigned short* XTp    = (unsigned short*)(base + off); off += XTB;
-    float* xBC_BC          = (float*)(base + off);          off += XBCBCB;
-    unsigned short* BTp    = (unsigned short*)(base + off); off += BTB;
-    unsigned short* Cbp    = (unsigned short*)(base + off); off += CBB;
-    unsigned short* Gp     = (unsigned short*)(base + off); off += GBYTES;
-    float* dtbuf           = (float*)(base + off);          off += DTB;
-    float* A_cum           = (float*)(base + off);          off += ACUMB;
-    unsigned short* statesT= (unsigned short*)(base + off); off += STB;
-    char*  T               = base + off;
-    unsigned short* xhi    = (unsigned short*)T;
-    unsigned short* xlo    = (unsigned short*)(T + XHB);
-    unsigned short* wbc_hi = (unsigned short*)(T + 2*XHB);
-    unsigned short* wbc_lo = (unsigned short*)(T + 2*XHB + WBCB);
-    unsigned short* w1b    = (unsigned short*)(T + 2*XHB + 2*WBCB);
-    float* bcpart          = (float*)w1b;
-    unsigned short* yb     = (unsigned short*)T;
-    unsigned short* w2b    = (unsigned short*)(T + YBB);
+    us* projb  = (us*)(base + off); off += PROJB;
+    float* projBC = (float*)(base + off); off += PROJBCB;
+    us* XTp    = (us*)(base + off); off += XTB;
+    float* xBC_BC = (float*)(base + off); off += XBCBCB;
+    us* BTp    = (us*)(base + off); off += BTB;
+    us* Cbp    = (us*)(base + off); off += CBB;
+    us* Gp     = (us*)(base + off); off += GBYTES;
+    float* dtbuf = (float*)(base + off); off += DTB;
+    float* A_cum = (float*)(base + off); off += ACUMB;
+    us* statesT = (us*)(base + off); off += STB;
+    char*  T   = base + off;
+    us* xhi    = (us*)T;
+    us* xlo    = (us*)(T + XHB);
+    us* wbc_hi = (us*)(T + 2*XHB);
+    us* wbc_lo = (us*)(T + 2*XHB + WBCB);
+    us* w1b    = (us*)(T + 2*XHB + 2*WBCB);
+    float* bcpart = (float*)w1b;
+    us* yb     = (us*)T;
+    us* w2b    = (us*)(T + YBB);
 
     {
         unsigned total_blocks = (unsigned)((N4A + N4B + N4C) / 256);
         prep_kernel<<<total_blocks, 256, 0, stream>>>(x, in_w, xhi, xlo, w1b, wbc_hi, wbc_lo);
     }
-    gemm_bf16<true><<<dim3(PROJ_PAD/128, TOK/128), 256, 0, stream>>>(xhi, HIDDEN, w1b, HIDDEN,
-                                                                     projb, PROJ_PAD, HIDDEN);
-    bc_splitk_mfma<<<dim3(NBCP/128, TOK/128, KSPL2), 256, 0, stream>>>(xhi, xlo, wbc_hi, wbc_lo, bcpart);
-    reduce_bc2<<<(unsigned)(((size_t)TOK*NBCP/4)/256), 256, 0, stream>>>(bcpart, dt_bias, projBC, dtbuf);
-    conv_fused<<<XBLK + TOK + W2BLK, 256, 0, stream>>>(projb, projBC, conv_w, conv_b, out_w,
-                                                       XTp, xBC_BC, BTp, Cbp, w2b);
-    cumsum_kernel<<<dim3(NC, NUM_HEADS, BATCH), 256, 0, stream>>>(dtbuf, A_log, A_cum);
-    g_kernel<<<dim3(NC, 36, BATCH), 256, 0, stream>>>(xBC_BC, Gp);
-    states_mfma<<<dim3(NC, NUM_HEADS, BATCH), 256, 0, stream>>>(XTp, BTp, dtbuf, A_cum, statesT);
+    mega_gemm1_bc<<<G1_BLOCKS + BC_BLOCKS, 256, 0, stream>>>(xhi, xlo, w1b, wbc_hi, wbc_lo,
+                                                             projb, bcpart);
+    mega_red_convxt<<<RED_BLOCKS + CXT_BLOCKS, 256, 0, stream>>>(bcpart, dt_bias, projb,
+                                                                 conv_w, conv_b,
+                                                                 projBC, dtbuf, XTp);
+    mega_convbc_cum_w2<<<CBC_BLOCKS + CUM_BLOCKS + W2_BLOCKS, 256, 0, stream>>>(
+        projBC, conv_w, conv_b, dtbuf, A_log, out_w, xBC_BC, BTp, Cbp, A_cum, w2b);
+    mega_states_g<<<ST_BLOCKS + GK_BLOCKS, 256, 0, stream>>>(XTp, BTp, dtbuf, A_cum, xBC_BC,
+                                                             statesT, Gp);
     recur_kernel<<<dim3(NUM_HEADS, BATCH, 4), 256, 0, stream>>>(A_cum, statesT);
     yscan_mfma<<<dim3(NC*4, NUM_HEADS, BATCH), 256, 0, stream>>>(Gp, Cbp, XTp, dtbuf, A_cum,
                                                                  statesT, Dvec, projb);
```

Result: no change. 702.7 us (-1.1%).
